# Kernel optimization log

Hardware: AMD Instinct MI355X
Metric: run time of the kernel (lower is better)

The kernel has to match this reference:

```python
import jax, jax.numpy as jnp
import numpy as np

N_NODES = 100000
N_EDGES = 1600000
NUM_FEATURES = 128


def setup_inputs() -> dict:
    key = jax.random.key(0)
    ks = jax.random.split(key, 10)
    x = jax.random.normal(ks[0], (N_NODES, NUM_FEATURES), dtype=jnp.float32)
    edge_index = jax.random.randint(ks[1], (2, N_EDGES), 0, N_NODES, dtype=jnp.int64)
    # conv1 MLP: Linear(num_features,128) -> ReLU -> Linear(128,128)
    s1 = 1.0 / np.sqrt(NUM_FEATURES)
    W1 = jax.random.uniform(ks[2], (NUM_FEATURES, 128), jnp.float32, -s1, s1)
    b1 = jax.random.uniform(ks[3], (128,), jnp.float32, -s1, s1)
    s2 = 1.0 / np.sqrt(128)
    W2 = jax.random.uniform(ks[4], (128, 128), jnp.float32, -s2, s2)
    b2 = jax.random.uniform(ks[5], (128,), jnp.float32, -s2, s2)
    # conv2 MLP: Linear(128,64) -> ReLU -> Linear(64,64)
    W3 = jax.random.uniform(ks[6], (128, 64), jnp.float32, -s2, s2)
    b3 = jax.random.uniform(ks[7], (64,), jnp.float32, -s2, s2)
    s3 = 1.0 / np.sqrt(64)
    W4 = jax.random.uniform(ks[8], (64, 64), jnp.float32, -s3, s3)
    b4 = jax.random.uniform(ks[9], (64,), jnp.float32, -s3, s3)
    return {"x": x, "edge_index": edge_index, "W1": W1, "b1": b1,
            "W2": W2, "b2": b2, "W3": W3, "b3": b3, "W4": W4, "b4": b4}


def _gin_conv(x, src, dst, Wa, ba, Wb, bb):
    # GINConv with eps=0: out = MLP(x + sum_{j->i} x_j)
    agg = jax.ops.segment_sum(x[src], dst, num_segments=N_NODES)
    h = x + agg
    h = jax.nn.relu(h @ Wa + ba)
    return h @ Wb + bb


def reference(x, edge_index, W1, b1, W2, b2, W3, b3, W4, b4):
    src, dst = edge_index[0], edge_index[1]
    h = jax.nn.relu(_gin_conv(x, src, dst, W1, b1, W2, b2))
    h = jax.nn.relu(_gin_conv(h, src, dst, W3, b3, W4, b4))
    return h
```

## Files before the change

kernel.cpp:

```cpp
#include <hip/hip_runtime.h>
#include <hip/hip_bf16.h>

#define NODES 100000
#define EDGES 1600000
#define NBINS ((NODES + 127) >> 7)
#define BINCAP 2560
#define PB_BLOCKS 256
#define PB_CHUNK ((EDGES + PB_BLOCKS - 1) / PB_BLOCKS)
#define CAST_BLOCKS 12500
#define WPREP_BLOCKS 176

typedef __bf16 bf16x8 __attribute__((ext_vector_type(8)));
typedef float f32x4 __attribute__((ext_vector_type(4)));

__device__ __forceinline__ unsigned short f2b(float f) {
  __hip_bfloat16 h = __float2bfloat16(f);
  return __builtin_bit_cast(unsigned short, h);
}
__device__ __forceinline__ float b_lo(unsigned u) { return __uint_as_float(u << 16); }
__device__ __forceinline__ float b_hi(unsigned u) { return __uint_as_float(u & 0xffff0000u); }

__global__ __launch_bounds__(256) void prep_count(
    const float4* __restrict__ x4, ushort4* __restrict__ xh4,
    const float* __restrict__ W1, const float* __restrict__ W2,
    const float* __restrict__ W3, const float* __restrict__ W4,
    unsigned short* __restrict__ Wt1, unsigned short* __restrict__ Wt2,
    unsigned short* __restrict__ Wt3, unsigned short* __restrict__ Wt4,
    int* __restrict__ cnt) {
  const int b = blockIdx.x;
  if (b < CAST_BLOCKS) {
    int i = b * 256 + threadIdx.x;
    float4 v = x4[i];
    ushort4 o;
    o.x = f2b(v.x); o.y = f2b(v.y); o.z = f2b(v.z); o.w = f2b(v.w);
    xh4[i] = o;
    return;
  }
  if (b < CAST_BLOCKS + WPREP_BLOCKS) {
    int i = (b - CAST_BLOCKS) * 256 + threadIdx.x;
    if (i < 16384) {
      int n = i >> 7, k = i & 127;
      Wt1[i] = f2b(W1[k * 128 + n]);
    } else if (i < 32768) {
      int j = i - 16384; int n = j >> 7, k = j & 127;
      Wt2[j] = f2b(W2[k * 128 + n]);
    } else if (i < 40960) {
      int j = i - 32768; int n = j >> 7, k = j & 127;
      Wt3[j] = f2b(W3[k * 64 + n]);
    } else if (i < 45056) {
      int j = i - 40960; int n = j >> 6, k = j & 63;
      Wt4[j] = f2b(W4[k * 64 + n]);
    }
    return;
  }
  for (int i = threadIdx.x; i < NBINS; i += 256) cnt[i] = 0;
}

__global__ __launch_bounds__(256) void bin_scatter(const int* __restrict__ src,
                                                   const int* __restrict__ dst,
                                                   int* __restrict__ cnt,
                                                   unsigned* __restrict__ coarse) {
  __shared__ int base[NBINS];
  __shared__ int h[NBINS];
  const int beg = blockIdx.x * PB_CHUNK;
  const int end = min(beg + PB_CHUNK, EDGES);
  for (int i = threadIdx.x; i < NBINS; i += 256) h[i] = 0;
  __syncthreads();
  for (int e = beg + threadIdx.x; e < end; e += 256)
    atomicAdd(&h[dst[e] >> 7], 1);
  __syncthreads();
  for (int i = threadIdx.x; i < NBINS; i += 256) {
    int c = h[i];
    if (c > 0) base[i] = atomicAdd(&cnt[i], c);
    h[i] = 0;
  }
  __syncthreads();
  for (int e = beg + threadIdx.x; e < end; e += 256) {
    int d = dst[e];
    int b = d >> 7;
    int pos = base[b] + atomicAdd(&h[b], 1);
    coarse[(size_t)b * BINCAP + pos] = (unsigned)src[e] | ((unsigned)(d & 127) << 17);
  }
}

__global__ __launch_bounds__(256) void bin_fine(const unsigned* __restrict__ coarse,
                                                const int* __restrict__ cnt,
                                                int2* __restrict__ rowpairs,
                                                int* __restrict__ bucket) {
  __shared__ unsigned ent[BINCAP];
  __shared__ unsigned obuf[BINCAP];
  __shared__ int deg[128];
  __shared__ int pre[128];
  const int b = blockIdx.x;
  const int t = threadIdx.x;
  const int s0 = b * BINCAP;
  const int nE = cnt[b];
  const int binBase = b << 7;

  if (t < 128) deg[t] = 0;
  __syncthreads();
  for (int i = t; i < nE; i += 256) {
    unsigned e = coarse[s0 + i];
    ent[i] = e;
    atomicAdd(&deg[e >> 17], 1);
  }
  __syncthreads();
  int v = 0;
  if (t < 128) {
    v = deg[t];
    pre[t] = v;
  }
  __syncthreads();
  for (int off = 1; off < 128; off <<= 1) {
    int u = (t >= off && t < 128) ? pre[t - off] : 0;
    __syncthreads();
    if (t < 128) pre[t] += u;
    __syncthreads();
  }
  if (t < 128) {
    int inc = pre[t];
    int ex = inc - v;
    if (binBase + t < NODES) rowpairs[binBase + t] = make_int2(s0 + ex, s0 + inc);
    deg[t] = ex;
  }
  __syncthreads();
  for (int i = t; i < nE; i += 256) {
    unsigned e = ent[i];
    int pos = atomicAdd(&deg[e >> 17], 1);
    obuf[pos] = e & 0x1FFFFu;
  }
  __syncthreads();
  for (int i = t; i < nE; i += 256) bucket[s0 + i] = (int)obuf[i];
}

__global__ __launch_bounds__(256) void gather_sum_bf16(
    const uint4* __restrict__ xq, const int2* __restrict__ rowpairs,
    const int* __restrict__ bucket, uint4* __restrict__ outq) {
  const int n = blockIdx.x * 4 + (threadIdx.x >> 6);
  if (n >= NODES) return;
  const int lane = threadIdx.x & 63;
  const int g = lane >> 4;
  const int fl = lane & 15;

  float a[8] = {0.f, 0.f, 0.f, 0.f, 0.f, 0.f, 0.f, 0.f};
  if (g == 0) {
    uint4 v = xq[(size_t)n * 16 + fl];
    a[0] = b_lo(v.x); a[1] = b_hi(v.x);
    a[2] = b_lo(v.y); a[3] = b_hi(v.y);
    a[4] = b_lo(v.z); a[5] = b_hi(v.z);
    a[6] = b_lo(v.w); a[7] = b_hi(v.w);
  }

  const int2 se = rowpairs[n];
  const int beg = se.x;
  const int end = se.y;
  for (int j = beg; j < end; j += 16) {
    int e0 = j + g, e1 = j + 4 + g, e2 = j + 8 + g, e3 = j + 12 + g;
    int i0 = (e0 < end) ? e0 : (end - 1);
    int i1 = (e1 < end) ? e1 : (end - 1);
    int i2 = (e2 < end) ? e2 : (end - 1);
    int i3 = (e3 < end) ? e3 : (end - 1);
    int s0 = bucket[i0], s1 = bucket[i1], s2 = bucket[i2], s3 = bucket[i3];
    uint4 v0 = xq[(size_t)s0 * 16 + fl];
    uint4 v1 = xq[(size_t)s1 * 16 + fl];
    uint4 v2 = xq[(size_t)s2 * 16 + fl];
    uint4 v3 = xq[(size_t)s3 * 16 + fl];
    float m0 = (e0 < end) ? 1.f : 0.f;
    float m1 = (e1 < end) ? 1.f : 0.f;
    float m2 = (e2 < end) ? 1.f : 0.f;
    float m3 = (e3 < end) ? 1.f : 0.f;
    a[0] = fmaf(b_lo(v0.x), m0, a[0]); a[1] = fmaf(b_hi(v0.x), m0, a[1]);
    a[2] = fmaf(b_lo(v0.y), m0, a[2]); a[3] = fmaf(b_hi(v0.y), m0, a[3]);
    a[4] = fmaf(b_lo(v0.z), m0, a[4]); a[5] = fmaf(b_hi(v0.z), m0, a[5]);
    a[6] = fmaf(b_lo(v0.w), m0, a[6]); a[7] = fmaf(b_hi(v0.w), m0, a[7]);
    a[0] = fmaf(b_lo(v1.x), m1, a[0]); a[1] = fmaf(b_hi(v1.x), m1, a[1]);
    a[2] = fmaf(b_lo(v1.y), m1, a[2]); a[3] = fmaf(b_hi(v1.y), m1, a[3]);
    a[4] = fmaf(b_lo(v1.z), m1, a[4]); a[5] = fmaf(b_hi(v1.z), m1, a[5]);
    a[6] = fmaf(b_lo(v1.w), m1, a[6]); a[7] = fmaf(b_hi(v1.w), m1, a[7]);
    a[0] = fmaf(b_lo(v2.x), m2, a[0]); a[1] = fmaf(b_hi(v2.x), m2, a[1]);
    a[2] = fmaf(b_lo(v2.y), m2, a[2]); a[3] = fmaf(b_hi(v2.y), m2, a[3]);
    a[4] = fmaf(b_lo(v2.z), m2, a[4]); a[5] = fmaf(b_hi(v2.z), m2, a[5]);
    a[6] = fmaf(b_lo(v2.w), m2, a[6]); a[7] = fmaf(b_hi(v2.w), m2, a[7]);
    a[0] = fmaf(b_lo(v3.x), m3, a[0]); a[1] = fmaf(b_hi(v3.x), m3, a[1]);
    a[2] = fmaf(b_lo(v3.y), m3, a[2]); a[3] = fmaf(b_hi(v3.y), m3, a[3]);
    a[4] = fmaf(b_lo(v3.z), m3, a[4]); a[5] = fmaf(b_hi(v3.z), m3, a[5]);
    a[6] = fmaf(b_lo(v3.w), m3, a[6]); a[7] = fmaf(b_hi(v3.w), m3, a[7]);
  }

#pragma unroll
  for (int k = 0; k < 8; k++) {
    a[k] += __shfl_xor(a[k], 16, 64);
    a[k] += __shfl_xor(a[k], 32, 64);
  }

  if (lane < 16) {
    uint4 o;
    o.x = ((unsigned)f2b(a[1]) << 16) | f2b(a[0]);
    o.y = ((unsigned)f2b(a[3]) << 16) | f2b(a[2]);
    o.z = ((unsigned)f2b(a[5]) << 16) | f2b(a[4]);
    o.w = ((unsigned)f2b(a[7]) << 16) | f2b(a[6]);
    outq[(size_t)n * 16 + fl] = o;
  }
}

template <int K, int N1, int N2, bool OUT_F32>
__global__ __launch_bounds__(256, 3) void mlp_fused(
    const unsigned short* __restrict__ A,
    const unsigned short* __restrict__ Wa, const float* __restrict__ ba,
    const unsigned short* __restrict__ Wb, const float* __restrict__ bb,
    void* __restrict__ Cout, int M) {
  constexpr int LDA = K + 8;
  constexpr int LWA = K + 8;
  constexpr int LWB = N1 + 8;
  constexpr int NT1 = N1 / 16, KB1 = K / 32;
  constexpr int NT2 = N2 / 16, KB2 = N1 / 32;
  constexpr int WSH = (N1 * LWA > N2 * LWB) ? N1 * LWA : N2 * LWB;
  __shared__ unsigned short S[64 * LDA];
  __shared__ unsigned short Wl[WSH];

  const int tid = threadIdx.x;
  const int wave = tid >> 6;
  const int lane = tid & 63;
  const int g = lane >> 4;
  const int fl = lane & 15;
  const int rowBase = blockIdx.x * 64;

  for (int i = tid; i < 64 * (K / 8); i += 256) {
    int r = i / (K / 8), c = i % (K / 8);
    uint4 v = make_uint4(0, 0, 0, 0);
    if (rowBase + r < M)
      v = ((const uint4*)A)[(size_t)(rowBase + r) * (K / 8) + c];
    *(uint4*)&S[r * LDA + c * 8] = v;
  }
  for (int i = tid; i < N1 * (K / 8); i += 256) {
    int n = i / (K / 8), c = i % (K / 8);
    *(uint4*)&Wl[n * LWA + c * 8] = *(const uint4*)&Wa[(size_t)n * K + c * 8];
  }
  __syncthreads();

  const int arow = wave * 16 + fl;

  f32x4 acc[NT1];
#pragma unroll
  for (int c = 0; c < NT1; c++) acc[c] = (f32x4){0.f, 0.f, 0.f, 0.f};
#pragma unroll
  for (int kb = 0; kb < KB1; kb++) {
    bf16x8 av = *(const bf16x8*)&S[arow * LDA + kb * 32 + g * 8];
#pragma unroll
    for (int c = 0; c < NT1; c++) {
      bf16x8 bv = *(const bf16x8*)&Wl[(c * 16 + fl) * LWA + kb * 32 + g * 8];
      acc[c] = __builtin_amdgcn_mfma_f32_16x16x32_bf16(av, bv, acc[c], 0, 0, 0);
    }
  }

#pragma unroll
  for (int c = 0; c < NT1; c++) {
    int col = c * 16 + fl;
    float bv = ba[col];
#pragma unroll
    for (int reg = 0; reg < 4; reg++) {
      int rloc = wave * 16 + g * 4 + reg;
      S[rloc * LDA + col] = f2b(fmaxf(acc[c][reg] + bv, 0.f));
    }
  }
  __syncthreads();

  for (int i = tid; i < N2 * (N1 / 8); i += 256) {
    int n = i / (N1 / 8), c = i % (N1 / 8);
    *(uint4*)&Wl[n * LWB + c * 8] = *(const uint4*)&Wb[(size_t)n * N1 + c * 8];
  }
  __syncthreads();

  f32x4 acc2[NT2];
#pragma unroll
  for (int c = 0; c < NT2; c++) acc2[c] = (f32x4){0.f, 0.f, 0.f, 0.f};
#pragma unroll
  for (int kb = 0; kb < KB2; kb++) {
    bf16x8 av = *(const bf16x8*)&S[arow * LDA + kb * 32 + g * 8];
#pragma unroll
    for (int c = 0; c < NT2; c++) {
      bf16x8 bv = *(const bf16x8*)&Wl[(c * 16 + fl) * LWB + kb * 32 + g * 8];
      acc2[c] = __builtin_amdgcn_mfma_f32_16x16x32_bf16(av, bv, acc2[c], 0, 0, 0);
    }
  }

#pragma unroll
  for (int c = 0; c < NT2; c++) {
    int col = c * 16 + fl;
    float bv = bb[col];
#pragma unroll
    for (int reg = 0; reg < 4; reg++) {
      int row = rowBase + wave * 16 + g * 4 + reg;
      if (row < M) {
        float v = fmaxf(acc2[c][reg] + bv, 0.f);
        if (OUT_F32)
          ((float*)Cout)[(size_t)row * N2 + col] = v;
        else
          ((unsigned short*)Cout)[(size_t)row * N2 + col] = f2b(v);
      }
    }
  }
}

extern "C" void kernel_launch(void* const* d_in, const int* in_sizes, int n_in,
                              void* d_out, int out_size, void* d_ws, size_t ws_size,
                              hipStream_t stream) {
  const float* x = (const float*)d_in[0];
  const int* ei = (const int*)d_in[1];
  const int* src = ei;
  const int* dst = ei + EDGES;
  const float* W1 = (const float*)d_in[2];
  const float* b1 = (const float*)d_in[3];
  const float* W2 = (const float*)d_in[4];
  const float* b2 = (const float*)d_in[5];
  const float* W3 = (const float*)d_in[6];
  const float* b3 = (const float*)d_in[7];
  const float* W4 = (const float*)d_in[8];
  const float* b4 = (const float*)d_in[9];
  float* out = (float*)d_out;

  char* ws = (char*)d_ws;
  unsigned short* xh = (unsigned short*)ws;
  unsigned short* hA = xh + (size_t)NODES * 128;
  unsigned short* hB = hA + (size_t)NODES * 128;
  unsigned short* Wt1 = hB + (size_t)NODES * 128;
  unsigned short* Wt2 = Wt1 + 128 * 128;
  unsigned short* Wt3 = Wt2 + 128 * 128;
  unsigned short* Wt4 = Wt3 + 64 * 128;
  int2* rowpairs = (int2*)(Wt4 + 64 * 64);
  int* cnt = (int*)(rowpairs + NODES);
  unsigned* coarse = (unsigned*)(cnt + 784);
  int* bucket = (int*)(coarse + (size_t)NBINS * BINCAP);

  const int nblocks4 = (NODES + 3) / 4;
  const int gblocks = (NODES + 63) / 64;

  prep_count<<<CAST_BLOCKS + WPREP_BLOCKS + 1, 256, 0, stream>>>(
      (const float4*)x, (ushort4*)xh, W1, W2, W3, W4, Wt1, Wt2, Wt3, Wt4, cnt);
  bin_scatter<<<PB_BLOCKS, 256, 0, stream>>>(src, dst, cnt, coarse);
  bin_fine<<<NBINS, 256, 0, stream>>>(coarse, cnt, rowpairs, bucket);

  gather_sum_bf16<<<nblocks4, 256, 0, stream>>>((const uint4*)xh, rowpairs, bucket,
                                                (uint4*)hA);
  mlp_fused<128, 128, 128, false><<<gblocks, 256, 0, stream>>>(
      hA, Wt1, b1, Wt2, b2, hB, NODES);
  gather_sum_bf16<<<nblocks4, 256, 0, stream>>>((const uint4*)hB, rowpairs, bucket,
                                                (uint4*)hA);
  mlp_fused<128, 64, 64, true><<<gblocks, 256, 0, stream>>>(
      hA, Wt3, b3, Wt4, b4, out, NODES);
}
```

Baseline: 328.4 us.

## Fuse neighbor gather-sum into MLP kernel, writing aggregates directly to LDS

```diff
diff --git a/kernel.cpp b/kernel.cpp
--- a/kernel.cpp
+++ b/kernel.cpp
@@ -133,79 +133,16 @@
   for (int i = t; i < nE; i += 256) bucket[s0 + i] = (int)obuf[i];
 }
 
-__global__ __launch_bounds__(256) void gather_sum_bf16(
+#define ACC8(r, m)                                                            \
+  a[0] = fmaf(b_lo(r.x), m, a[0]); a[1] = fmaf(b_hi(r.x), m, a[1]);           \
+  a[2] = fmaf(b_lo(r.y), m, a[2]); a[3] = fmaf(b_hi(r.y), m, a[3]);           \
+  a[4] = fmaf(b_lo(r.z), m, a[4]); a[5] = fmaf(b_hi(r.z), m, a[5]);           \
+  a[6] = fmaf(b_lo(r.w), m, a[6]); a[7] = fmaf(b_hi(r.w), m, a[7]);
+
+template <int K, int N1, int N2, bool OUT_F32>
+__global__ __launch_bounds__(256, 3) void gin_layer(
     const uint4* __restrict__ xq, const int2* __restrict__ rowpairs,
-    const int* __restrict__ bucket, uint4* __restrict__ outq) {
-  const int n = blockIdx.x * 4 + (threadIdx.x >> 6);
-  if (n >= NODES) return;
-  const int lane = threadIdx.x & 63;
-  const int g = lane >> 4;
-  const int fl = lane & 15;
-
-  float a[8] = {0.f, 0.f, 0.f, 0.f, 0.f, 0.f, 0.f, 0.f};
-  if (g == 0) {
-    uint4 v = xq[(size_t)n * 16 + fl];
-    a[0] = b_lo(v.x); a[1] = b_hi(v.x);
-    a[2] = b_lo(v.y); a[3] = b_hi(v.y);
-    a[4] = b_lo(v.z); a[5] = b_hi(v.z);
-    a[6] = b_lo(v.w); a[7] = b_hi(v.w);
-  }
-
-  const int2 se = rowpairs[n];
-  const int beg = se.x;
-  const int end = se.y;
-  for (int j = beg; j < end; j += 16) {
-    int e0 = j + g, e1 = j + 4 + g, e2 = j + 8 + g, e3 = j + 12 + g;
-    int i0 = (e0 < end) ? e0 : (end - 1);
-    int i1 = (e1 < end) ? e1 : (end - 1);
-    int i2 = (e2 < end) ? e2 : (end - 1);
-    int i3 = (e3 < end) ? e3 : (end - 1);
-    int s0 = bucket[i0], s1 = bucket[i1], s2 = bucket[i2], s3 = bucket[i3];
-    uint4 v0 = xq[(size_t)s0 * 16 + fl];
-    uint4 v1 = xq[(size_t)s1 * 16 + fl];
-    uint4 v2 = xq[(size_t)s2 * 16 + fl];
-    uint4 v3 = xq[(size_t)s3 * 16 + fl];
-    float m0 = (e0 < end) ? 1.f : 0.f;
-    float m1 = (e1 < end) ? 1.f : 0.f;
-    float m2 = (e2 < end) ? 1.f : 0.f;
-    float m3 = (e3 < end) ? 1.f : 0.f;
-    a[0] = fmaf(b_lo(v0.x), m0, a[0]); a[1] = fmaf(b_hi(v0.x), m0, a[1]);
-    a[2] = fmaf(b_lo(v0.y), m0, a[2]); a[3] = fmaf(b_hi(v0.y), m0, a[3]);
-    a[4] = fmaf(b_lo(v0.z), m0, a[4]); a[5] = fmaf(b_hi(v0.z), m0, a[5]);
-    a[6] = fmaf(b_lo(v0.w), m0, a[6]); a[7] = fmaf(b_hi(v0.w), m0, a[7]);
-    a[0] = fmaf(b_lo(v1.x), m1, a[0]); a[1] = fmaf(b_hi(v1.x), m1, a[1]);
-    a[2] = fmaf(b_lo(v1.y), m1, a[2]); a[3] = fmaf(b_hi(v1.y), m1, a[3]);
-    a[4] = fmaf(b_lo(v1.z), m1, a[4]); a[5] = fmaf(b_hi(v1.z), m1, a[5]);
-    a[6] = fmaf(b_lo(v1.w), m1, a[6]); a[7] = fmaf(b_hi(v1.w), m1, a[7]);
-    a[0] = fmaf(b_lo(v2.x), m2, a[0]); a[1] = fmaf(b_hi(v2.x), m2, a[1]);
-    a[2] = fmaf(b_lo(v2.y), m2, a[2]); a[3] = fmaf(b_hi(v2.y), m2, a[3]);
-    a[4] = fmaf(b_lo(v2.z), m2, a[4]); a[5] = fmaf(b_hi(v2.z), m2, a[5]);
-    a[6] = fmaf(b_lo(v2.w), m2, a[6]); a[7] = fmaf(b_hi(v2.w), m2, a[7]);
-    a[0] = fmaf(b_lo(v3.x), m3, a[0]); a[1] = fmaf(b_hi(v3.x), m3, a[1]);
-    a[2] = fmaf(b_lo(v3.y), m3, a[2]); a[3] = fmaf(b_hi(v3.y), m3, a[3]);
-    a[4] = fmaf(b_lo(v3.z), m3, a[4]); a[5] = fmaf(b_hi(v3.z), m3, a[5]);
-    a[6] = fmaf(b_lo(v3.w), m3, a[6]); a[7] = fmaf(b_hi(v3.w), m3, a[7]);
-  }
-
-#pragma unroll
-  for (int k = 0; k < 8; k++) {
-    a[k] += __shfl_xor(a[k], 16, 64);
-    a[k] += __shfl_xor(a[k], 32, 64);
-  }
-
-  if (lane < 16) {
-    uint4 o;
-    o.x = ((unsigned)f2b(a[1]) << 16) | f2b(a[0]);
-    o.y = ((unsigned)f2b(a[3]) << 16) | f2b(a[2]);
-    o.z = ((unsigned)f2b(a[5]) << 16) | f2b(a[4]);
-    o.w = ((unsigned)f2b(a[7]) << 16) | f2b(a[6]);
-    outq[(size_t)n * 16 + fl] = o;
-  }
-}
-
-template <int K, int N1, int N2, bool OUT_F32>
-__global__ __launch_bounds__(256, 3) void mlp_fused(
-    const unsigned short* __restrict__ A,
+    const int* __restrict__ bucket,
     const unsigned short* __restrict__ Wa, const float* __restrict__ ba,
     const unsigned short* __restrict__ Wb, const float* __restrict__ bb,
     void* __restrict__ Cout, int M) {
@@ -225,16 +162,55 @@
   const int fl = lane & 15;
   const int rowBase = blockIdx.x * 64;
 
-  for (int i = tid; i < 64 * (K / 8); i += 256) {
-    int r = i / (K / 8), c = i % (K / 8);
-    uint4 v = make_uint4(0, 0, 0, 0);
-    if (rowBase + r < M)
-      v = ((const uint4*)A)[(size_t)(rowBase + r) * (K / 8) + c];
-    *(uint4*)&S[r * LDA + c * 8] = v;
-  }
   for (int i = tid; i < N1 * (K / 8); i += 256) {
     int n = i / (K / 8), c = i % (K / 8);
     *(uint4*)&Wl[n * LWA + c * 8] = *(const uint4*)&Wa[(size_t)n * K + c * 8];
+  }
+
+  for (int p = 0; p < 4; p++) {
+    const int rloc = wave * 16 + p * 4 + g;
+    const int n = rowBase + rloc;
+    float a[8] = {0.f, 0.f, 0.f, 0.f, 0.f, 0.f, 0.f, 0.f};
+    if (n < M) {
+      uint4 v = xq[(size_t)n * 16 + fl];
+      a[0] = b_lo(v.x); a[1] = b_hi(v.x);
+      a[2] = b_lo(v.y); a[3] = b_hi(v.y);
+      a[4] = b_lo(v.z); a[5] = b_hi(v.z);
+      a[6] = b_lo(v.w); a[7] = b_hi(v.w);
+      const int2 se = rowpairs[n];
+      const int beg = se.x, end = se.y;
+      for (int j = beg; j < end; j += 8) {
+        int i0 = j,     i1 = min(j + 1, end - 1), i2 = min(j + 2, end - 1),
+            i3 = min(j + 3, end - 1), i4 = min(j + 4, end - 1),
+            i5 = min(j + 5, end - 1), i6 = min(j + 6, end - 1),
+            i7 = min(j + 7, end - 1);
+        int s0 = bucket[i0], s1 = bucket[i1], s2 = bucket[i2], s3 = bucket[i3];
+        int s4 = bucket[i4], s5 = bucket[i5], s6 = bucket[i6], s7 = bucket[i7];
+        uint4 r0 = xq[(size_t)s0 * 16 + fl];
+        uint4 r1 = xq[(size_t)s1 * 16 + fl];
+        uint4 r2 = xq[(size_t)s2 * 16 + fl];
+        uint4 r3 = xq[(size_t)s3 * 16 + fl];
+        uint4 r4 = xq[(size_t)s4 * 16 + fl];
+        uint4 r5 = xq[(size_t)s5 * 16 + fl];
+        uint4 r6 = xq[(size_t)s6 * 16 + fl];
+        uint4 r7 = xq[(size_t)s7 * 16 + fl];
+        float m1 = (j + 1 < end) ? 1.f : 0.f;
+        float m2 = (j + 2 < end) ? 1.f : 0.f;
+        float m3 = (j + 3 < end) ? 1.f : 0.f;
+        float m4 = (j + 4 < end) ? 1.f : 0.f;
+        float m5 = (j + 5 < end) ? 1.f : 0.f;
+        float m6 = (j + 6 < end) ? 1.f : 0.f;
+        float m7 = (j + 7 < end) ? 1.f : 0.f;
+        ACC8(r0, 1.f) ACC8(r1, m1) ACC8(r2, m2) ACC8(r3, m3)
+        ACC8(r4, m4) ACC8(r5, m5) ACC8(r6, m6) ACC8(r7, m7)
+      }
+    }
+    uint4 o;
+    o.x = ((unsigned)f2b(a[1]) << 16) | f2b(a[0]);
+    o.y = ((unsigned)f2b(a[3]) << 16) | f2b(a[2]);
+    o.z = ((unsigned)f2b(a[5]) << 16) | f2b(a[4]);
+    o.w = ((unsigned)f2b(a[7]) << 16) | f2b(a[6]);
+    *(uint4*)&S[rloc * LDA + fl * 8] = o;
   }
   __syncthreads();
 
@@ -321,8 +297,7 @@
 
   char* ws = (char*)d_ws;
   unsigned short* xh = (unsigned short*)ws;
-  unsigned short* hA = xh + (size_t)NODES * 128;
-  unsigned short* hB = hA + (size_t)NODES * 128;
+  unsigned short* hB = xh + (size_t)NODES * 128;
   unsigned short* Wt1 = hB + (size_t)NODES * 128;
   unsigned short* Wt2 = Wt1 + 128 * 128;
   unsigned short* Wt3 = Wt2 + 128 * 128;
@@ -332,7 +307,6 @@
   unsigned* coarse = (unsigned*)(cnt + 784);
   int* bucket = (int*)(coarse + (size_t)NBINS * BINCAP);
 
-  const int nblocks4 = (NODES + 3) / 4;
   const int gblocks = (NODES + 63) / 64;
 
   prep_count<<<CAST_BLOCKS + WPREP_BLOCKS + 1, 256, 0, stream>>>(
@@ -340,12 +314,8 @@
   bin_scatter<<<PB_BLOCKS, 256, 0, stream>>>(src, dst, cnt, coarse);
   bin_fine<<<NBINS, 256, 0, stream>>>(coarse, cnt, rowpairs, bucket);
 
-  gather_sum_bf16<<<nblocks4, 256, 0, stream>>>((const uint4*)xh, rowpairs, bucket,
-                                                (uint4*)hA);
-  mlp_fused<128, 128, 128, false><<<gblocks, 256, 0, stream>>>(
-      hA, Wt1, b1, Wt2, b2, hB, NODES);
-  gather_sum_bf16<<<nblocks4, 256, 0, stream>>>((const uint4*)hB, rowpairs, bucket,
-                                                (uint4*)hA);
-  mlp_fused<128, 64, 64, true><<<gblocks, 256, 0, stream>>>(
-      hA, Wt3, b3, Wt4, b4, out, NODES);
-}
+  gin_layer<128, 128, 128, false><<<gblocks, 256, 0, stream>>>(
+      (const uint4*)xh, rowpairs, bucket, Wt1, b1, Wt2, b2, hB, NODES);
+  gin_layer<128, 64, 64, true><<<gblocks, 256, 0, stream>>>(
+      (const uint4*)hB, rowpairs, bucket, Wt3, b3, Wt4, b4, out, NODES);
+}
```

Result: faster. 315.2 us (-4.0%).
